# Kernel optimization log

Measured on AMD Instinct MI355X. Metric: run time of the kernel, lower is better.

## Reference

```python
import jax, jax.numpy as jnp
import numpy as np

B, N, D, H, DK, DV, HID = 4, 16384, 512, 8, 64, 64, 2048
LN_EPS = 1e-5   # torch nn.LayerNorm default
ATTN_EPS = 1e-6 # eps passed to LinearMultiHeadAttention


def _ln(h, g, b):
    m = jnp.mean(h, axis=-1, keepdims=True)
    v = jnp.mean(jnp.square(h - m), axis=-1, keepdims=True)
    return (h - m) * jax.lax.rsqrt(v + LN_EPS) * g + b


def setup_inputs() -> dict:
    key = jax.random.key(0)
    ks = jax.random.split(key, 8)
    w = lambda k, *sh: (jax.random.normal(k, sh, jnp.float32) * 0.02)
    return {
        "x": jax.random.normal(ks[0], (B, N, D), jnp.float32),
        "ln1_g": jnp.ones((D,), jnp.float32), "ln1_b": jnp.zeros((D,), jnp.float32),
        "Wq": w(ks[1], D, H * DK), "bq": jnp.zeros((H * DK,), jnp.float32),
        "Wk": w(ks[2], D, H * DK), "bk": jnp.zeros((H * DK,), jnp.float32),
        "Wv": w(ks[3], D, H * DV), "bv": jnp.zeros((H * DV,), jnp.float32),
        "Wo": w(ks[4], H * DV, D), "bo": jnp.zeros((D,), jnp.float32),
        "ln2_g": jnp.ones((D,), jnp.float32), "ln2_b": jnp.zeros((D,), jnp.float32),
        "W1": w(ks[5], D, HID), "b1": jnp.zeros((HID,), jnp.float32),
        "W2": w(ks[6], HID, D), "b2": jnp.zeros((D,), jnp.float32),
    }


def reference(x, ln1_g, ln1_b, Wq, bq, Wk, bk, Wv, bv, Wo, bo,
              ln2_g, ln2_b, W1, b1, W2, b2):
    # pre-LN (zero-width label concat is a no-op in label_embedded mode)
    h = _ln(x, ln1_g, ln1_b)                         # [B,N,D]
    q = (h @ Wq + bq).reshape(B, N, H, DK)
    k = (h @ Wk + bk).reshape(B, N, H, DK)
    v = (h @ Wv + bv).reshape(B, N, H, DV)
    # linear attention: phi = elu + 1 feature map, O(N) non-causal form
    pq = jax.nn.elu(q) + 1.0
    pk = jax.nn.elu(k) + 1.0
    kv = jnp.einsum('bnhd,bnhm->bhdm', pk, v)        # [B,H,DK,DV]
    ksum = jnp.sum(pk, axis=1)                       # [B,H,DK]
    z = 1.0 / (jnp.einsum('bnhd,bhd->bnh', pq, ksum) + ATTN_EPS)
    attn = jnp.einsum('bnhd,bhdm->bnhm', pq, kv) * z[..., None]
    attn = attn.reshape(B, N, H * DV) @ Wo + bo      # output projection
    h = h + attn                                     # residual 1
    h2 = _ln(h, ln2_g, ln2_b)
    dense = jax.nn.gelu(h2 @ W1 + b1) @ W2 + b2      # MLP, gelu activation
    return h2 + dense                                # residual 2
```

## Files before the change

### kernel.cpp

```cpp
#include <hip/hip_runtime.h>
#include <stdint.h>

#define BB   4
#define NN   16384
#define HH   8
#define DD   512
#define HIDN 2048
#define ROWST (BB * NN)

using short8 = __attribute__((ext_vector_type(8))) short;
using f32x4  = __attribute__((ext_vector_type(4))) float;

__device__ __forceinline__ float bf2f(uint16_t h) {
  union { uint32_t u; float f; } v; v.u = ((uint32_t)h) << 16; return v.f;
}
__device__ __forceinline__ uint16_t f2bf(float f) {
  union { float f; uint32_t u; } v; v.f = f;
  return (uint16_t)((v.u + 0x7FFFu + ((v.u >> 16) & 1u)) >> 16);
}
__device__ __forceinline__ float gelu_f(float x) {
  const float t1 = x * x;
  const float inner = __builtin_fmaf(0.044715f * t1, x, x);
  const float e = __expf(-1.5957691216f * inner);
  return x * __builtin_amdgcn_rcpf(1.f + e);
}
__device__ __forceinline__ void cp16(const uint16_t* g, uint16_t* l) {
  __builtin_amdgcn_global_load_lds((const __attribute__((address_space(1))) void*)g,
                                   (__attribute__((address_space(3))) void*)l, 16, 0, 0);
}
__device__ __forceinline__ int swz(int row, int col) {
  return row * 64 + (col ^ (row & 56));
}

template <int E>
__launch_bounds__(256)
__global__ void gemm_bt(const uint16_t* __restrict__ A, const uint16_t* __restrict__ BT,
                        const float* __restrict__ bias, const uint16_t* __restrict__ res,
                        void* __restrict__ outp, int M, int N, int K) {
  __shared__ __align__(16) uint16_t S[128 * 128];
  uint16_t* As = S;
  uint16_t* Bs = S + 128 * 64;
  const int tid = threadIdx.x;
  const int lane = tid & 63, wave = tid >> 6;
  const int l15 = lane & 15, l4 = lane >> 4;
  const int m0 = blockIdx.y * 128, n0 = blockIdx.x * 128;
  const int wm = (wave >> 1) * 64, wn = (wave & 1) * 64;

  f32x4 acc[4][4];
#pragma unroll
  for (int i = 0; i < 4; ++i)
#pragma unroll
    for (int j = 0; j < 4; ++j) acc[i][j] = (f32x4){0.f, 0.f, 0.f, 0.f};

  const int srow = tid >> 3;
  const int skc  = ((tid & 7) ^ (srow & 7)) * 8;
  const uint16_t* ga = A  + (size_t)(m0 + srow) * K + skc;
  const uint16_t* gb = BT + (size_t)(n0 + srow) * K + skc;

  for (int kb = 0; kb < K; kb += 64) {
    __syncthreads();
#pragma unroll
    for (int i = 0; i < 4; ++i) {
      cp16(ga + (size_t)i * 32 * K + kb, &As[(i * 256 + wave * 64) * 8]);
      cp16(gb + (size_t)i * 32 * K + kb, &Bs[(i * 256 + wave * 64) * 8]);
    }
    __syncthreads();
#pragma unroll
    for (int kk = 0; kk < 64; kk += 32) {
      short8 af[4], bfr[4];
#pragma unroll
      for (int i = 0; i < 4; ++i)
        af[i] = *(const short8*)&As[(wm + i * 16 + l15) * 64 +
                                    ((((kk >> 3) + l4) ^ (l15 & 7)) * 8)];
#pragma unroll
      for (int j = 0; j < 4; ++j)
        bfr[j] = *(const short8*)&Bs[(wn + j * 16 + l15) * 64 +
                                     ((((kk >> 3) + l4) ^ (l15 & 7)) * 8)];
#pragma unroll
      for (int i = 0; i < 4; ++i)
#pragma unroll
        for (int j = 0; j < 4; ++j)
          acc[i][j] = __builtin_amdgcn_mfma_f32_16x16x32_bf16(af[i], bfr[j], acc[i][j], 0, 0, 0);
    }
  }

  __syncthreads();
#pragma unroll
  for (int i = 0; i < 4; ++i)
#pragma unroll
    for (int r = 0; r < 4; ++r) {
      const int lrow = wm + i * 16 + l4 * 4 + r;
#pragma unroll
      for (int j = 0; j < 4; ++j) {
        const int lcol = wn + j * 16 + l15;
        float v = acc[i][j][r] + bias[n0 + lcol];
        if (E == 5) {
          if (n0 + lcol < 1024) v = v > 0.f ? v + 1.f : __expf(v);
        } else if (E == 3) {
          v = gelu_f(v);
        }
        S[lrow * 128 + ((((lcol >> 3) ^ (lrow >> 2)) & 15) * 8) + (lcol & 7)] = f2bf(v);
      }
    }
  __syncthreads();

  uint16_t* outb = (uint16_t*)outp;
  float* outf = (float*)outp;
  const int rr = tid >> 4;
  const int cb = tid & 15;
#pragma unroll
  for (int p = 0; p < 8; ++p) {
    const int lrow = p * 16 + rr;
    const int row = m0 + lrow;
    const int col0 = n0 + cb * 8;
    const uint4 d = *(const uint4*)&S[lrow * 128 + ((cb ^ (lrow >> 2)) & 15) * 8];
    if (E == 5) {
      const size_t off = (size_t)(col0 >> 9) * ((size_t)ROWST * DD) +
                         (size_t)row * DD + (col0 & 511);
      *(uint4*)&outb[off] = d;
    } else if (E == 1 || E == 3) {
      *(uint4*)&outb[(size_t)row * N + col0] = d;
    } else {
      const size_t idx = (size_t)row * N + col0;
      const uint4 rd = *(const uint4*)&res[idx];
      float a[8];
      a[0] = bf2f((uint16_t)(d.x & 0xffff)) + bf2f((uint16_t)(rd.x & 0xffff));
      a[1] = bf2f((uint16_t)(d.x >> 16))    + bf2f((uint16_t)(rd.x >> 16));
      a[2] = bf2f((uint16_t)(d.y & 0xffff)) + bf2f((uint16_t)(rd.y & 0xffff));
      a[3] = bf2f((uint16_t)(d.y >> 16))    + bf2f((uint16_t)(rd.y >> 16));
      a[4] = bf2f((uint16_t)(d.z & 0xffff)) + bf2f((uint16_t)(rd.z & 0xffff));
      a[5] = bf2f((uint16_t)(d.z >> 16))    + bf2f((uint16_t)(rd.z >> 16));
      a[6] = bf2f((uint16_t)(d.w & 0xffff)) + bf2f((uint16_t)(rd.w & 0xffff));
      a[7] = bf2f((uint16_t)(d.w >> 16))    + bf2f((uint16_t)(rd.w >> 16));
      if (E == 2) {
        uint4 o;
        o.x = (uint32_t)f2bf(a[0]) | ((uint32_t)f2bf(a[1]) << 16);
        o.y = (uint32_t)f2bf(a[2]) | ((uint32_t)f2bf(a[3]) << 16);
        o.z = (uint32_t)f2bf(a[4]) | ((uint32_t)f2bf(a[5]) << 16);
        o.w = (uint32_t)f2bf(a[6]) | ((uint32_t)f2bf(a[7]) << 16);
        *(uint4*)&outb[idx] = o;
      } else {
        *(float4*)&outf[idx]     = (float4){a[0], a[1], a[2], a[3]};
        *(float4*)&outf[idx + 4] = (float4){a[4], a[5], a[6], a[7]};
      }
    }
  }
}

template <int BFIN>
__launch_bounds__(256)
__global__ void ln_kernel(const void* __restrict__ inp, const float* __restrict__ gam,
                          const float* __restrict__ bet, uint16_t* __restrict__ out) {
  const int row = blockIdx.x * 4 + (threadIdx.x >> 6);
  const int lane = threadIdx.x & 63;
  const size_t base = (size_t)row * DD + lane * 8;
  float x[8];
  if (BFIN) {
    const uint4 u = *(const uint4*)((const uint16_t*)inp + base);
    x[0] = bf2f((uint16_t)(u.x & 0xffff)); x[1] = bf2f((uint16_t)(u.x >> 16));
    x[2] = bf2f((uint16_t)(u.y & 0xffff)); x[3] = bf2f((uint16_t)(u.y >> 16));
    x[4] = bf2f((uint16_t)(u.z & 0xffff)); x[5] = bf2f((uint16_t)(u.z >> 16));
    x[6] = bf2f((uint16_t)(u.w & 0xffff)); x[7] = bf2f((uint16_t)(u.w >> 16));
  } else {
    const float* f = (const float*)inp + base;
    const float4 a = *(const float4*)f;
    const float4 b = *(const float4*)(f + 4);
    x[0]=a.x; x[1]=a.y; x[2]=a.z; x[3]=a.w; x[4]=b.x; x[5]=b.y; x[6]=b.z; x[7]=b.w;
  }
  float s = 0.f, s2 = 0.f;
#pragma unroll
  for (int j = 0; j < 8; ++j) { s += x[j]; s2 += x[j] * x[j]; }
#pragma unroll
  for (int off = 32; off; off >>= 1) { s += __shfl_xor(s, off, 64); s2 += __shfl_xor(s2, off, 64); }
  const float m = s * (1.f / DD);
  const float rs = rsqrtf(s2 * (1.f / DD) - m * m + 1e-5f);
  uint16_t o[8];
#pragma unroll
  for (int j = 0; j < 8; ++j) {
    const int col = lane * 8 + j;
    o[j] = f2bf((x[j] - m) * rs * gam[col] + bet[col]);
  }
  uint4 w;
  w.x = (uint32_t)o[0] | ((uint32_t)o[1] << 16);
  w.y = (uint32_t)o[2] | ((uint32_t)o[3] << 16);
  w.z = (uint32_t)o[4] | ((uint32_t)o[5] << 16);
  w.w = (uint32_t)o[6] | ((uint32_t)o[7] << 16);
  *(uint4*)(out + base) = w;
}

__launch_bounds__(256)
__global__ void transpose_bf(const float* __restrict__ in, uint16_t* __restrict__ out,
                             int R, int C) {
  __shared__ float tile[32][33];
  const int tx = threadIdx.x, ty = threadIdx.y;
  const int c0 = blockIdx.x * 32, r0 = blockIdx.y * 32;
#pragma unroll
  for (int i = 0; i < 32; i += 8)
    tile[ty + i][tx] = in[(size_t)(r0 + ty + i) * C + (c0 + tx)];
  __syncthreads();
#pragma unroll
  for (int i = 0; i < 32; i += 8)
    out[(size_t)(c0 + ty + i) * R + (r0 + tx)] = f2bf(tile[tx][ty + i]);
}

__global__ void concat_bias(const float* __restrict__ bq, const float* __restrict__ bk,
                            const float* __restrict__ bv, float* __restrict__ o) {
  const int t = blockIdx.x * 256 + threadIdx.x;
  if (t < 512) o[t] = bq[t];
  else if (t < 1024) o[t] = bk[t - 512];
  else if (t < 1536) o[t] = bv[t - 1024];
}

__launch_bounds__(256)
__global__ void kv_mfma(const uint16_t* __restrict__ pk, const uint16_t* __restrict__ v,
                        float* __restrict__ kvp, float* __restrict__ ksp) {
  __shared__ __align__(16) uint16_t sT[4][2][64 * 64];
  __shared__ float ksred[64];
  const int bh = blockIdx.x, b = bh >> 3, h = bh & 7;
  const int t = threadIdx.x, lane = t & 63, w = t >> 6;
  const int l15 = lane & 15, l4 = lane >> 4;
  if (t < 64) ksred[t] = 0.f;
  __syncthreads();

  f32x4 acc[4][4];
#pragma unroll
  for (int i = 0; i < 4; ++i)
#pragma unroll
    for (int j = 0; j < 4; ++j) acc[i][j] = (f32x4){0.f, 0.f, 0.f, 0.f};
  float ks[4] = {0.f, 0.f, 0.f, 0.f};

  const int rl = lane >> 3, cl = (lane & 7) * 8;
  for (int sc = 0; sc < 4; ++sc) {
    const int nbase = blockIdx.y * 1024 + w * 256 + sc * 64;
#pragma unroll
    for (int ro = 0; ro < 8; ++ro) {
      const int n = ro * 8 + rl;
      const size_t gofs = ((size_t)(b * NN + nbase + n) * HH + h) * 64 + cl;
      const short8 pv = *(const short8*)(pk + gofs);
      const short8 vv = *(const short8*)(v + gofs);
#pragma unroll
      for (int j = 0; j < 8; ++j) {
        sT[w][0][swz(cl + j, n)] = (uint16_t)pv[j];
        sT[w][1][swz(cl + j, n)] = (uint16_t)vv[j];
      }
    }
#pragma unroll
    for (int kk = 0; kk < 64; kk += 32) {
      short8 af[4], bfr[4];
#pragma unroll
      for (int i = 0; i < 4; ++i)
        af[i] = *(const short8*)&sT[w][0][swz(i * 16 + l15, kk + l4 * 8)];
#pragma unroll
      for (int j = 0; j < 4; ++j)
        bfr[j] = *(const short8*)&sT[w][1][swz(j * 16 + l15, kk + l4 * 8)];
#pragma unroll
      for (int i = 0; i < 4; ++i) {
#pragma unroll
        for (int e = 0; e < 8; ++e) ks[i] += bf2f((uint16_t)af[i][e]);
#pragma unroll
        for (int j = 0; j < 4; ++j)
          acc[i][j] = __builtin_amdgcn_mfma_f32_16x16x32_bf16(af[i], bfr[j], acc[i][j], 0, 0, 0);
      }
    }
  }
#pragma unroll
  for (int i = 0; i < 4; ++i) {
    float s = ks[i];
    s += __shfl_xor(s, 16, 64); s += __shfl_xor(s, 32, 64);
    if (l4 == 0) atomicAdd(&ksred[i * 16 + l15], s);
  }
  __syncthreads();
  float* red = (float*)&sT[0][0][0];
  if (w > 0) {
#pragma unroll
    for (int i = 0; i < 4; ++i)
#pragma unroll
      for (int r = 0; r < 4; ++r)
#pragma unroll
        for (int j = 0; j < 4; ++j)
          red[(w - 1) * 4096 + (i * 16 + l4 * 4 + r) * 64 + j * 16 + l15] = acc[i][j][r];
  }
  __syncthreads();
  if (w == 0) {
    float* dst = kvp + ((size_t)bh * 16 + blockIdx.y) * 4096;
#pragma unroll
    for (int i = 0; i < 4; ++i)
#pragma unroll
      for (int r = 0; r < 4; ++r)
#pragma unroll
        for (int j = 0; j < 4; ++j) {
          const int e = (i * 16 + l4 * 4 + r) * 64 + j * 16 + l15;
          dst[e] = acc[i][j][r] + red[e] + red[4096 + e] + red[8192 + e];
        }
  }
  if (t < 64) ksp[((size_t)bh * 16 + blockIdx.y) * 64 + t] = ksred[t];
}

__launch_bounds__(256)
__global__ void kv_reduce(const float* __restrict__ kvp, const float* __restrict__ ksp,
                          float* __restrict__ kv, float* __restrict__ ksum) {
  const int bh = blockIdx.x;
  if (blockIdx.y == 16) {
    if (threadIdx.x < 64) {
      float s = 0.f;
      for (int c = 0; c < 16; ++c) s += ksp[((size_t)bh * 16 + c) * 64 + threadIdx.x];
      ksum[bh * 64 + threadIdx.x] = s;
    }
    return;
  }
  const int e = blockIdx.y * 256 + threadIdx.x;
  float s = 0.f;
  for (int c = 0; c < 16; ++c) s += kvp[((size_t)bh * 16 + c) * 4096 + e];
  kv[(size_t)bh * 4096 + e] = s;
}

__launch_bounds__(256)
__global__ void attn_mfma(const uint16_t* __restrict__ pq, const float* __restrict__ kv,
                          const float* __restrict__ ksum, uint16_t* __restrict__ attn) {
  __shared__ __align__(16) uint16_t kvT[64 * 64];
  __shared__ float ksS[64];
  __shared__ float denS[4][64];
  const int bh = blockIdx.x, b = bh >> 3, h = bh & 7;
  const int t = threadIdx.x, lane = t & 63, w = t >> 6;
  const int l15 = lane & 15, l4 = lane >> 4;
  const float* kvb = kv + (size_t)bh * 4096;
#pragma unroll
  for (int u = 0; u < 16; ++u) {
    const int e = u * 256 + t;
    kvT[swz(e & 63, e >> 6)] = f2bf(kvb[e]);
  }
  if (t < 64) ksS[t] = ksum[bh * 64 + t];
  __syncthreads();

  float ksr[16];
#pragma unroll
  for (int kk2 = 0; kk2 < 2; ++kk2) {
    const float4 k0 = *(const float4*)&ksS[kk2 * 32 + l4 * 8];
    const float4 k1 = *(const float4*)&ksS[kk2 * 32 + l4 * 8 + 4];
    ksr[kk2 * 8 + 0] = k0.x; ksr[kk2 * 8 + 1] = k0.y; ksr[kk2 * 8 + 2] = k0.z; ksr[kk2 * 8 + 3] = k0.w;
    ksr[kk2 * 8 + 4] = k1.x; ksr[kk2 * 8 + 5] = k1.y; ksr[kk2 * 8 + 6] = k1.z; ksr[kk2 * 8 + 7] = k1.w;
  }
  short8 bfrg[2][4];
#pragma unroll
  for (int kk2 = 0; kk2 < 2; ++kk2)
#pragma unroll
    for (int j = 0; j < 4; ++j)
      bfrg[kk2][j] = *(const short8*)&kvT[swz(j * 16 + l15, kk2 * 32 + l4 * 8)];

  const int n0w = blockIdx.y * 256 + w * 64;
  f32x4 acc[4][4];
#pragma unroll
  for (int i = 0; i < 4; ++i)
#pragma unroll
    for (int j = 0; j < 4; ++j) acc[i][j] = (f32x4){0.f, 0.f, 0.f, 0.f};
  float den[4] = {0.f, 0.f, 0.f, 0.f};

#pragma unroll
  for (int i = 0; i < 4; ++i) {
    const int n = n0w + i * 16 + l15;
    const size_t abase = ((size_t)(b * NN + n) * HH + h) * 64 + l4 * 8;
#pragma unroll
    for (int kk2 = 0; kk2 < 2; ++kk2) {
      const short8 af = *(const short8*)(pq + abase + kk2 * 32);
#pragma unroll
      for (int e = 0; e < 8; ++e) den[i] += bf2f((uint16_t)af[e]) * ksr[kk2 * 8 + e];
#pragma unroll
      for (int j = 0; j < 4; ++j)
        acc[i][j] = __builtin_amdgcn_mfma_f32_16x16x32_bf16(af, bfrg[kk2][j], acc[i][j], 0, 0, 0);
    }
  }
#pragma unroll
  for (int i = 0; i < 4; ++i) {
    float s = den[i];
    s += __shfl_xor(s, 16, 64); s += __shfl_xor(s, 32, 64);
    if (l4 == 0) denS[w][i * 16 + l15] = s;
  }
#pragma unroll
  for (int i = 0; i < 4; ++i)
#pragma unroll
    for (int r = 0; r < 4; ++r) {
      const float z = 1.f / (denS[w][i * 16 + l4 * 4 + r] + 1e-6f);
      const int n = n0w + i * 16 + l4 * 4 + r;
      const size_t ob = ((size_t)(b * NN + n) * HH + h) * 64;
#pragma unroll
      for (int j = 0; j < 4; ++j)
        attn[ob + j * 16 + l15] = f2bf(acc[i][j][r] * z);
    }
}

extern "C" void kernel_launch(void* const* d_in, const int* in_sizes, int n_in,
                              void* d_out, int out_size, void* d_ws, size_t ws_size,
                              hipStream_t stream) {
  (void)in_sizes; (void)n_in; (void)out_size;
  const float* x    = (const float*)d_in[0];
  const float* ln1g = (const float*)d_in[1];
  const float* ln1b = (const float*)d_in[2];
  const float* Wq   = (const float*)d_in[3];
  const float* bq   = (const float*)d_in[4];
  const float* Wk   = (const float*)d_in[5];
  const float* bk   = (const float*)d_in[6];
  const float* Wv   = (const float*)d_in[7];
  const float* bv   = (const float*)d_in[8];
  const float* Wo   = (const float*)d_in[9];
  const float* bo   = (const float*)d_in[10];
  const float* ln2g = (const float*)d_in[11];
  const float* ln2b = (const float*)d_in[12];
  const float* W1   = (const float*)d_in[13];
  const float* b1   = (const float*)d_in[14];
  const float* W2   = (const float*)d_in[15];
  const float* b2   = (const float*)d_in[16];

  if (ws_size < 409000000ULL) return;

  char* p = (char*)d_ws;
  auto alloc = [&](size_t bytes) -> char* {
    char* r = p; p += (bytes + 255) & ~(size_t)255; return r;
  };
  uint16_t* Hb  = (uint16_t*)alloc((size_t)ROWST * DD * 2);
  uint16_t* PQ  = (uint16_t*)alloc((size_t)ROWST * DD * 2);
  uint16_t* PK  = (uint16_t*)alloc((size_t)ROWST * DD * 2);
  uint16_t* PV  = (uint16_t*)alloc((size_t)ROWST * DD * 2);
  uint16_t* U   = (uint16_t*)alloc((size_t)32768 * HIDN * 2);
  uint16_t* WqkvT = (uint16_t*)alloc((size_t)1536 * DD * 2);
  uint16_t* WoT = (uint16_t*)alloc((size_t)DD * DD * 2);
  uint16_t* W1T = (uint16_t*)alloc((size_t)HIDN * DD * 2);
  uint16_t* W2T = (uint16_t*)alloc((size_t)DD * HIDN * 2);
  float*    bqkv = (float*)alloc(1536 * 4);
  float* KVP = (float*)U;
  float* KSP = KVP + 512 * 4096;
  float* KV  = KSP + 512 * 64;
  float* KS  = KV + 32 * 4096;

  const dim3 tb(32, 8);
  transpose_bf<<<dim3(16, 16), tb, 0, stream>>>(Wq, WqkvT, DD, DD);
  transpose_bf<<<dim3(16, 16), tb, 0, stream>>>(Wk, WqkvT + 512 * 512, DD, DD);
  transpose_bf<<<dim3(16, 16), tb, 0, stream>>>(Wv, WqkvT + 2 * 512 * 512, DD, DD);
  transpose_bf<<<dim3(16, 16), tb, 0, stream>>>(Wo, WoT, DD, DD);
  transpose_bf<<<dim3(64, 16), tb, 0, stream>>>(W1, W1T, DD, HIDN);
  transpose_bf<<<dim3(16, 64), tb, 0, stream>>>(W2, W2T, HIDN, DD);
  concat_bias<<<6, 256, 0, stream>>>(bq, bk, bv, bqkv);

  ln_kernel<0><<<ROWST / 4, 256, 0, stream>>>(x, ln1g, ln1b, Hb);
  gemm_bt<5><<<dim3(12, 512), 256, 0, stream>>>(Hb, WqkvT, bqkv, nullptr, PQ, ROWST, 1536, DD);
  kv_mfma<<<dim3(32, 16), 256, 0, stream>>>(PK, PV, KVP, KSP);
  kv_reduce<<<dim3(32, 17), 256, 0, stream>>>(KVP, KSP, KV, KS);
  attn_mfma<<<dim3(32, 64), 256, 0, stream>>>(PQ, KV, KS, PV);
  gemm_bt<2><<<dim3(4, 512), 256, 0, stream>>>(PV, WoT, bo, Hb, PK, ROWST, DD, DD);
  ln_kernel<1><<<ROWST / 4, 256, 0, stream>>>(PK, ln2g, ln2b, PQ);
  for (int c = 0; c < 2; ++c) {
    const uint16_t* h2c = PQ + (size_t)c * 32768 * DD;
    gemm_bt<3><<<dim3(16, 256), 256, 0, stream>>>(h2c, W1T, b1, nullptr, U, 32768, HIDN, DD);
    gemm_bt<4><<<dim3(4, 256), 256, 0, stream>>>(U, W2T, b2, h2c,
        (float*)d_out + (size_t)c * 32768 * DD, 32768, DD, HIDN);
  }
}
```

Baseline: 1.037 ms.

## Replace GEMM with 256x128 triple-buffered pipelined kernel and XCD-aware tile remap

The 128x128 single-buffered GEMM is replaced by a 512-thread, 256x128-tile kernel that keeps three LDS stages and issues the global-to-LDS loads two k-steps ahead, using explicit waitcnt and barriers. MFMA blocks get raised wave priority, and workgroup IDs are remapped so consecutive tiles land on the same XCD for better L2 reuse. The goal is to hide load latency behind MFMA work and cut synchronisation per k-step. In exchange it uses much more LDS (144KB per block) and relies on hand-placed vmcnt counts being correct.

```diff
diff --git a/kernel.cpp b/kernel.cpp
--- a/kernel.cpp
+++ b/kernel.cpp
@@ -33,67 +33,97 @@
 }
 
 template <int E>
-__launch_bounds__(256)
-__global__ void gemm_bt(const uint16_t* __restrict__ A, const uint16_t* __restrict__ BT,
+__launch_bounds__(512, 2)
+__global__ void gemm256(const uint16_t* __restrict__ A, const uint16_t* __restrict__ BT,
                         const float* __restrict__ bias, const uint16_t* __restrict__ res,
                         void* __restrict__ outp, int M, int N, int K) {
-  __shared__ __align__(16) uint16_t S[128 * 128];
-  uint16_t* As = S;
-  uint16_t* Bs = S + 128 * 64;
+  __shared__ __align__(16) uint16_t S[3 * 24576];
   const int tid = threadIdx.x;
   const int lane = tid & 63, wave = tid >> 6;
   const int l15 = lane & 15, l4 = lane >> 4;
-  const int m0 = blockIdx.y * 128, n0 = blockIdx.x * 128;
   const int wm = (wave >> 1) * 64, wn = (wave & 1) * 64;
 
+  const int gx = gridDim.x;
+  const int nwg = gx * gridDim.y;
+  const int orig = blockIdx.y * gx + blockIdx.x;
+  const int q = nwg >> 3, r = nwg & 7;
+  const int xcd = orig & 7, off = orig >> 3;
+  const int tile = (xcd < r ? xcd * (q + 1) : r * (q + 1) + (xcd - r) * q) + off;
+  const int tn = tile % gx, tm = tile / gx;
+  const int m0 = tm * 256, n0 = tn * 128;
+
+  uint16_t *A0 = S,             *B0 = S + 16384;
+  uint16_t *A1 = S + 24576,     *B1 = S + 40960;
+  uint16_t *A2 = S + 49152,     *B2 = S + 65536;
+
+  const int srow = tid >> 3;
+  const int scb  = (tid & 7) ^ (srow & 7);
+  const uint16_t* ga = A  + (size_t)(m0 + srow) * K + scb * 8;
+  const uint16_t* gb = BT + (size_t)(n0 + srow) * K + scb * 8;
+  auto stage = [&](uint16_t* Ad, uint16_t* Bd, int kb) {
+#pragma unroll
+    for (int r2 = 0; r2 < 4; ++r2)
+      cp16(ga + (size_t)r2 * 64 * K + kb, Ad + (r2 * 64 + wave * 8) * 64);
+#pragma unroll
+    for (int r2 = 0; r2 < 2; ++r2)
+      cp16(gb + (size_t)r2 * 64 * K + kb, Bd + (r2 * 64 + wave * 8) * 64);
+  };
+
   f32x4 acc[4][4];
 #pragma unroll
   for (int i = 0; i < 4; ++i)
 #pragma unroll
     for (int j = 0; j < 4; ++j) acc[i][j] = (f32x4){0.f, 0.f, 0.f, 0.f};
 
-  const int srow = tid >> 3;
-  const int skc  = ((tid & 7) ^ (srow & 7)) * 8;
-  const uint16_t* ga = A  + (size_t)(m0 + srow) * K + skc;
-  const uint16_t* gb = BT + (size_t)(n0 + srow) * K + skc;
-
-  for (int kb = 0; kb < K; kb += 64) {
-    __syncthreads();
-#pragma unroll
-    for (int i = 0; i < 4; ++i) {
-      cp16(ga + (size_t)i * 32 * K + kb, &As[(i * 256 + wave * 64) * 8]);
-      cp16(gb + (size_t)i * 32 * K + kb, &Bs[(i * 256 + wave * 64) * 8]);
-    }
-    __syncthreads();
-#pragma unroll
-    for (int kk = 0; kk < 64; kk += 32) {
-      short8 af[4], bfr[4];
+  const int NT = K >> 6;
+  stage(A0, B0, 0);
+  stage(A1, B1, 64);
+  asm volatile("s_waitcnt vmcnt(6)" ::: "memory");
+  __builtin_amdgcn_s_barrier();
+  asm volatile("" ::: "memory");
+
+  for (int t = 0; t < NT; ++t) {
+    short8 af[2][4], bfr[2][4];
+#pragma unroll
+    for (int h = 0; h < 2; ++h) {
 #pragma unroll
       for (int i = 0; i < 4; ++i)
-        af[i] = *(const short8*)&As[(wm + i * 16 + l15) * 64 +
-                                    ((((kk >> 3) + l4) ^ (l15 & 7)) * 8)];
+        af[h][i] = *(const short8*)&A0[(wm + i * 16 + l15) * 64 +
+                                       (((h * 4 + l4) ^ (l15 & 7)) * 8)];
 #pragma unroll
       for (int j = 0; j < 4; ++j)
-        bfr[j] = *(const short8*)&Bs[(wn + j * 16 + l15) * 64 +
-                                     ((((kk >> 3) + l4) ^ (l15 & 7)) * 8)];
+        bfr[h][j] = *(const short8*)&B0[(wn + j * 16 + l15) * 64 +
+                                        (((h * 4 + l4) ^ (l15 & 7)) * 8)];
+    }
+    if (t + 2 < NT) stage(A2, B2, (t + 2) << 6);
+#pragma unroll
+    for (int h = 0; h < 2; ++h) {
+      __builtin_amdgcn_s_setprio(1);
 #pragma unroll
       for (int i = 0; i < 4; ++i)
 #pragma unroll
         for (int j = 0; j < 4; ++j)
-          acc[i][j] = __builtin_amdgcn_mfma_f32_16x16x32_bf16(af[i], bfr[j], acc[i][j], 0, 0, 0);
-    }
-  }
-
-  __syncthreads();
+          acc[i][j] = __builtin_amdgcn_mfma_f32_16x16x32_bf16(af[h][i], bfr[h][j],
+                                                              acc[i][j], 0, 0, 0);
+      __builtin_amdgcn_s_setprio(0);
+    }
+    if (t + 2 < NT) asm volatile("s_waitcnt vmcnt(6) lgkmcnt(0)" ::: "memory");
+    else            asm volatile("s_waitcnt vmcnt(0) lgkmcnt(0)" ::: "memory");
+    __builtin_amdgcn_s_barrier();
+    asm volatile("" ::: "memory");
+    uint16_t* tA = A0; A0 = A1; A1 = A2; A2 = tA;
+    uint16_t* tB = B0; B0 = B1; B1 = B2; B2 = tB;
+  }
+
 #pragma unroll
   for (int i = 0; i < 4; ++i)
 #pragma unroll
-    for (int r = 0; r < 4; ++r) {
-      const int lrow = wm + i * 16 + l4 * 4 + r;
+    for (int rg = 0; rg < 4; ++rg) {
+      const int lrow = wm + i * 16 + l4 * 4 + rg;
 #pragma unroll
       for (int j = 0; j < 4; ++j) {
         const int lcol = wn + j * 16 + l15;
-        float v = acc[i][j][r] + bias[n0 + lcol];
+        float v = acc[i][j][rg] + bias[n0 + lcol];
         if (E == 5) {
           if (n0 + lcol < 1024) v = v > 0.f ? v + 1.f : __expf(v);
         } else if (E == 3) {
@@ -110,14 +140,14 @@
   const int cb = tid & 15;
 #pragma unroll
   for (int p = 0; p < 8; ++p) {
-    const int lrow = p * 16 + rr;
+    const int lrow = p * 32 + rr;
     const int row = m0 + lrow;
     const int col0 = n0 + cb * 8;
     const uint4 d = *(const uint4*)&S[lrow * 128 + ((cb ^ (lrow >> 2)) & 15) * 8];
     if (E == 5) {
-      const size_t off = (size_t)(col0 >> 9) * ((size_t)ROWST * DD) +
-                         (size_t)row * DD + (col0 & 511);
-      *(uint4*)&outb[off] = d;
+      const size_t offs = (size_t)(col0 >> 9) * ((size_t)ROWST * DD) +
+                          (size_t)row * DD + (col0 & 511);
+      *(uint4*)&outb[offs] = d;
     } else if (E == 1 || E == 3) {
       *(uint4*)&outb[(size_t)row * N + col0] = d;
     } else {
@@ -441,16 +471,16 @@
   concat_bias<<<6, 256, 0, stream>>>(bq, bk, bv, bqkv);
 
   ln_kernel<0><<<ROWST / 4, 256, 0, stream>>>(x, ln1g, ln1b, Hb);
-  gemm_bt<5><<<dim3(12, 512), 256, 0, stream>>>(Hb, WqkvT, bqkv, nullptr, PQ, ROWST, 1536, DD);
+  gemm256<5><<<dim3(12, 256), 512, 0, stream>>>(Hb, WqkvT, bqkv, nullptr, PQ, ROWST, 1536, DD);
   kv_mfma<<<dim3(32, 16), 256, 0, stream>>>(PK, PV, KVP, KSP);
   kv_reduce<<<dim3(32, 17), 256, 0, stream>>>(KVP, KSP, KV, KS);
   attn_mfma<<<dim3(32, 64), 256, 0, stream>>>(PQ, KV, KS, PV);
-  gemm_bt<2><<<dim3(4, 512), 256, 0, stream>>>(PV, WoT, bo, Hb, PK, ROWST, DD, DD);
+  gemm256<2><<<dim3(4, 256), 512, 0, stream>>>(PV, WoT, bo, Hb, PK, ROWST, DD, DD);
   ln_kernel<1><<<ROWST / 4, 256, 0, stream>>>(PK, ln2g, ln2b, PQ);
   for (int c = 0; c < 2; ++c) {
     const uint16_t* h2c = PQ + (size_t)c * 32768 * DD;
-    gemm_bt<3><<<dim3(16, 256), 256, 0, stream>>>(h2c, W1T, b1, nullptr, U, 32768, HIDN, DD);
-    gemm_bt<4><<<dim3(4, 256), 256, 0, stream>>>(U, W2T, b2, h2c,
+    gemm256<3><<<dim3(16, 128), 512, 0, stream>>>(h2c, W1T, b1, nullptr, U, 32768, HIDN, DD);
+    gemm256<4><<<dim3(4, 128), 512, 0, stream>>>(U, W2T, b2, h2c,
         (float*)d_out + (size_t)c * 32768 * DD, 32768, DD, HIDN);
   }
 }
```

New measurement: 980.0 us. 5.5% less time.

## Replace 128x128 GEMM with 256x256 double-buffered ping-pong MFMA kernel

Applied to the files above, without the earlier changes.

Replaces the 128x128-tile, 4-wave GEMM with a 256x256-tile, 8-wave kernel. It double-buffers global-to-LDS loads in half-K phases interleaved with MFMA bursts under s_setprio and explicit barriers, and remaps workgroup IDs so tiles are grouped in chunks of eight. The larger tile raises arithmetic intensity per LDS byte, and the software pipeline is meant to hide global load latency behind compute. It uses 128 KB of LDS and many accumulator registers, which could limit occupancy, and the hand-tuned waitcnt scheme depends on K being a multiple of 128.

```diff
diff --git a/kernel.cpp b/kernel.cpp
--- a/kernel.cpp
+++ b/kernel.cpp
@@ -33,91 +33,154 @@
 }
 
 template <int E>
-__launch_bounds__(256)
-__global__ void gemm_bt(const uint16_t* __restrict__ A, const uint16_t* __restrict__ BT,
+__launch_bounds__(512, 2)
+__global__ void gemm256(const uint16_t* __restrict__ A, const uint16_t* __restrict__ BT,
                         const float* __restrict__ bias, const uint16_t* __restrict__ res,
                         void* __restrict__ outp, int M, int N, int K) {
-  __shared__ __align__(16) uint16_t S[128 * 128];
-  uint16_t* As = S;
-  uint16_t* Bs = S + 128 * 64;
+  __shared__ __align__(16) uint16_t S[65536];
   const int tid = threadIdx.x;
   const int lane = tid & 63, wave = tid >> 6;
   const int l15 = lane & 15, l4 = lane >> 4;
-  const int m0 = blockIdx.y * 128, n0 = blockIdx.x * 128;
-  const int wm = (wave >> 1) * 64, wn = (wave & 1) * 64;
-
-  f32x4 acc[4][4];
-#pragma unroll
-  for (int i = 0; i < 4; ++i)
+  const int wm = (wave >> 2) * 128, wn = (wave & 3) * 64;
+
+  const int gx = gridDim.x;
+  const int nwg = gx * gridDim.y;
+  const int orig = blockIdx.y * gx + blockIdx.x;
+  const int cpx = nwg >> 3;
+  const int tile = (orig & 7) * cpx + (orig >> 3);
+  const int tn = tile % gx, tm = tile / gx;
+  const int m0 = tm * 256, n0 = tn * 256;
+
+  const int bsw = (tid & 7) ^ ((tid >> 3) & 7);
+  const int row_lo = ((tid >> 3) << 1) + (bsw >> 2);
+  const int c8 = (bsw & 3) * 8;
+  const uint16_t* pA = A  + (size_t)(m0 + row_lo) * K + c8;
+  const uint16_t* pB = BT + (size_t)(n0 + row_lo) * K + c8;
+  const size_t rstep = (size_t)128 * K;
+  const int dstw = wave * 512;
+
+  const int pbF = (((l15 & 1) << 2) | l4) ^ (l15 >> 1);
+  const int abase = wm * 32 + (l15 >> 1) * 64 + pbF * 8;
+  const int bbase = 16384 + wn * 32 + (l15 >> 1) * 64 + pbF * 8;
+
+  auto stageA = [&](int buf, int kh, int kb) {
+    uint16_t* d = S + buf * 32768 + kh * 8192 + dstw;
+    const uint16_t* s = pA + kb + kh * 32;
+    cp16(s, d);
+    cp16(s + rstep, d + 4096);
+  };
+  auto stageB = [&](int buf, int kh, int kb) {
+    uint16_t* d = S + buf * 32768 + 16384 + kh * 8192 + dstw;
+    const uint16_t* s = pB + kb + kh * 32;
+    cp16(s, d);
+    cp16(s + rstep, d + 4096);
+  };
+
+  f32x4 acc[8][4];
+#pragma unroll
+  for (int i = 0; i < 8; ++i)
 #pragma unroll
     for (int j = 0; j < 4; ++j) acc[i][j] = (f32x4){0.f, 0.f, 0.f, 0.f};
-
-  const int srow = tid >> 3;
-  const int skc  = ((tid & 7) ^ (srow & 7)) * 8;
-  const uint16_t* ga = A  + (size_t)(m0 + srow) * K + skc;
-  const uint16_t* gb = BT + (size_t)(n0 + srow) * K + skc;
-
-  for (int kb = 0; kb < K; kb += 64) {
-    __syncthreads();
-#pragma unroll
-    for (int i = 0; i < 4; ++i) {
-      cp16(ga + (size_t)i * 32 * K + kb, &As[(i * 256 + wave * 64) * 8]);
-      cp16(gb + (size_t)i * 32 * K + kb, &Bs[(i * 256 + wave * 64) * 8]);
-    }
-    __syncthreads();
-#pragma unroll
-    for (int kk = 0; kk < 64; kk += 32) {
-      short8 af[4], bfr[4];
-#pragma unroll
-      for (int i = 0; i < 4; ++i)
-        af[i] = *(const short8*)&As[(wm + i * 16 + l15) * 64 +
-                                    ((((kk >> 3) + l4) ^ (l15 & 7)) * 8)];
-#pragma unroll
-      for (int j = 0; j < 4; ++j)
-        bfr[j] = *(const short8*)&Bs[(wn + j * 16 + l15) * 64 +
-                                     ((((kk >> 3) + l4) ^ (l15 & 7)) * 8)];
-#pragma unroll
-      for (int i = 0; i < 4; ++i)
-#pragma unroll
-        for (int j = 0; j < 4; ++j)
-          acc[i][j] = __builtin_amdgcn_mfma_f32_16x16x32_bf16(af[i], bfr[j], acc[i][j], 0, 0, 0);
-    }
-  }
-
-  __syncthreads();
-#pragma unroll
-  for (int i = 0; i < 4; ++i)
-#pragma unroll
-    for (int r = 0; r < 4; ++r) {
-      const int lrow = wm + i * 16 + l4 * 4 + r;
+  short8 bf[4];
+
+  const int NT = K >> 6;
+  stageA(0, 0, 0);  stageB(0, 0, 0);
+  stageA(0, 1, 0);  stageB(0, 1, 0);
+  stageA(1, 0, 64); stageB(1, 0, 64);
+  asm volatile("s_waitcnt vmcnt(4)" ::: "memory");
+  __builtin_amdgcn_s_barrier();
+  asm volatile("" ::: "memory");
+
+#define PHASE(BUF, MH, KH, RB, PRE, POST)                                        \
+  {                                                                              \
+    short8 af[4];                                                                \
+    _Pragma("unroll")                                                            \
+    for (int f = 0; f < 4; ++f)                                                  \
+      af[f] = *(const short8*)&S[(BUF)*32768 + (KH)*8192 + (MH)*2048 + abase + f*512]; \
+    if (RB) {                                                                    \
+      _Pragma("unroll")                                                          \
+      for (int j = 0; j < 4; ++j)                                                \
+        bf[j] = *(const short8*)&S[(BUF)*32768 + (KH)*8192 + bbase + j*512];     \
+    }                                                                            \
+    PRE;                                                                         \
+    asm volatile("" ::: "memory");                                               \
+    __builtin_amdgcn_s_barrier();                                                \
+    asm volatile("s_waitcnt lgkmcnt(0)" ::: "memory");                           \
+    __builtin_amdgcn_sched_barrier(0);                                           \
+    __builtin_amdgcn_s_setprio(1);                                               \
+    _Pragma("unroll")                                                            \
+    for (int i = 0; i < 4; ++i)                                                  \
+      _Pragma("unroll")                                                          \
+      for (int j = 0; j < 4; ++j)                                                \
+        acc[(MH)*4 + i][j] = __builtin_amdgcn_mfma_f32_16x16x32_bf16(af[i], bf[j], acc[(MH)*4 + i][j], 0, 0, 0); \
+    __builtin_amdgcn_s_setprio(0);                                               \
+    __builtin_amdgcn_sched_barrier(0);                                           \
+    POST;                                                                        \
+    asm volatile("" ::: "memory");                                               \
+    __builtin_amdgcn_s_barrier();                                                \
+    asm volatile("" ::: "memory");                                               \
+  }
+
+  for (int t2 = 0; t2 < NT; t2 += 2) {
+    {
+      const int t = t2;
+      const int kb1 = (t + 1) << 6, kb2 = (t + 2) << 6;
+      PHASE(0, 0, 0, 1, if (t + 1 < NT) stageA(1, 1, kb1), {});
+      PHASE(0, 1, 0, 0, if (t + 1 < NT) stageB(1, 1, kb1), {});
+      PHASE(0, 0, 1, 1, if (t + 2 < NT) stageA(0, 0, kb2), {});
+      PHASE(0, 1, 1, 0, if (t + 2 < NT) stageB(0, 0, kb2),
+            if (t + 2 < NT) { asm volatile("s_waitcnt vmcnt(4)" ::: "memory"); }
+            else            { asm volatile("s_waitcnt vmcnt(0)" ::: "memory"); });
+    }
+    {
+      const int t = t2 + 1;
+      const int kb1 = (t + 1) << 6, kb2 = (t + 2) << 6;
+      PHASE(1, 0, 0, 1, if (t + 1 < NT) stageA(0, 1, kb1), {});
+      PHASE(1, 1, 0, 0, if (t + 1 < NT) stageB(0, 1, kb1), {});
+      PHASE(1, 0, 1, 1, if (t + 2 < NT) stageA(1, 0, kb2), {});
+      PHASE(1, 1, 1, 0, if (t + 2 < NT) stageB(1, 0, kb2),
+            if (t + 2 < NT) { asm volatile("s_waitcnt vmcnt(4)" ::: "memory"); }
+            else            { asm volatile("s_waitcnt vmcnt(0)" ::: "memory"); });
+    }
+  }
+#undef PHASE
+
+  __syncthreads();
+  const float bj[4] = {bias[n0 + wn + l15], bias[n0 + wn + 16 + l15],
+                       bias[n0 + wn + 32 + l15], bias[n0 + wn + 48 + l15]};
+#pragma unroll
+  for (int mf = 0; mf < 8; ++mf)
+#pragma unroll
+    for (int rg = 0; rg < 4; ++rg) {
+      const int lrow = wm + mf * 16 + l4 * 4 + rg;
 #pragma unroll
       for (int j = 0; j < 4; ++j) {
         const int lcol = wn + j * 16 + l15;
-        float v = acc[i][j][r] + bias[n0 + lcol];
+        float v = acc[mf][j][rg] + bj[j];
         if (E == 5) {
           if (n0 + lcol < 1024) v = v > 0.f ? v + 1.f : __expf(v);
         } else if (E == 3) {
           v = gelu_f(v);
         }
-        S[lrow * 128 + ((((lcol >> 3) ^ (lrow >> 2)) & 15) * 8) + (lcol & 7)] = f2bf(v);
+        S[lrow * 256 + ((((lcol >> 3) ^ lrow) & 31) * 8) + (lcol & 7)] = f2bf(v);
       }
     }
   __syncthreads();
 
   uint16_t* outb = (uint16_t*)outp;
   float* outf = (float*)outp;
-  const int rr = tid >> 4;
-  const int cb = tid & 15;
-#pragma unroll
-  for (int p = 0; p < 8; ++p) {
+  const int rr = tid >> 5;
+  const int cb = tid & 31;
+#pragma unroll
+  for (int p = 0; p < 16; ++p) {
     const int lrow = p * 16 + rr;
     const int row = m0 + lrow;
     const int col0 = n0 + cb * 8;
-    const uint4 d = *(const uint4*)&S[lrow * 128 + ((cb ^ (lrow >> 2)) & 15) * 8];
+    const uint4 d = *(const uint4*)&S[lrow * 256 + ((cb ^ lrow) & 31) * 8];
     if (E == 5) {
-      const size_t off = (size_t)(col0 >> 9) * ((size_t)ROWST * DD) +
-                         (size_t)row * DD + (col0 & 511);
-      *(uint4*)&outb[off] = d;
+      const size_t offs = (size_t)(col0 >> 9) * ((size_t)ROWST * DD) +
+                          (size_t)row * DD + (col0 & 511);
+      *(uint4*)&outb[offs] = d;
     } else if (E == 1 || E == 3) {
       *(uint4*)&outb[(size_t)row * N + col0] = d;
     } else {
@@ -441,16 +504,16 @@
   concat_bias<<<6, 256, 0, stream>>>(bq, bk, bv, bqkv);
 
   ln_kernel<0><<<ROWST / 4, 256, 0, stream>>>(x, ln1g, ln1b, Hb);
-  gemm_bt<5><<<dim3(12, 512), 256, 0, stream>>>(Hb, WqkvT, bqkv, nullptr, PQ, ROWST, 1536, DD);
+  gemm256<5><<<dim3(6, 256), 512, 0, stream>>>(Hb, WqkvT, bqkv, nullptr, PQ, ROWST, 1536, DD);
   kv_mfma<<<dim3(32, 16), 256, 0, stream>>>(PK, PV, KVP, KSP);
   kv_reduce<<<dim3(32, 17), 256, 0, stream>>>(KVP, KSP, KV, KS);
   attn_mfma<<<dim3(32, 64), 256, 0, stream>>>(PQ, KV, KS, PV);
-  gemm_bt<2><<<dim3(4, 512), 256, 0, stream>>>(PV, WoT, bo, Hb, PK, ROWST, DD, DD);
+  gemm256<2><<<dim3(2, 256), 512, 0, stream>>>(PV, WoT, bo, Hb, PK, ROWST, DD, DD);
   ln_kernel<1><<<ROWST / 4, 256, 0, stream>>>(PK, ln2g, ln2b, PQ);
   for (int c = 0; c < 2; ++c) {
     const uint16_t* h2c = PQ + (size_t)c * 32768 * DD;
-    gemm_bt<3><<<dim3(16, 256), 256, 0, stream>>>(h2c, W1T, b1, nullptr, U, 32768, HIDN, DD);
-    gemm_bt<4><<<dim3(4, 256), 256, 0, stream>>>(U, W2T, b2, h2c,
+    gemm256<3><<<dim3(8, 128), 512, 0, stream>>>(h2c, W1T, b1, nullptr, U, 32768, HIDN, DD);
+    gemm256<4><<<dim3(2, 128), 512, 0, stream>>>(U, W2T, b2, h2c,
         (float*)d_out + (size_t)c * 32768 * DD, 32768, DD, HIDN);
   }
 }
```

New measurement: 959.2 us. 1.08x faster.

## Replace GEMM with 256x128 double-buffered tile kernel and remapped block order

Applied to the files above, without the earlier changes.

Replaces the 128x128 single-buffered GEMM with a 256x128 tile kernel that double-buffers 32-wide K slices in LDS, so the next slice is loaded while MFMAs run on the current one. Each wave now holds a 128x64 accumulator block, raising register pressure. Launch bounds ask for two blocks per CU. Block indices are permuted across groups of eight, likely to improve L2 locality across XCDs. The epilogue is staged through LDS in two halves with bias preloaded into registers.

```diff
diff --git a/kernel.cpp b/kernel.cpp
--- a/kernel.cpp
+++ b/kernel.cpp
@@ -33,117 +33,139 @@
 }
 
 template <int E>
-__launch_bounds__(256)
-__global__ void gemm_bt(const uint16_t* __restrict__ A, const uint16_t* __restrict__ BT,
+__launch_bounds__(256, 2)
+__global__ void gemm256(const uint16_t* __restrict__ A, const uint16_t* __restrict__ BT,
                         const float* __restrict__ bias, const uint16_t* __restrict__ res,
                         void* __restrict__ outp, int M, int N, int K) {
-  __shared__ __align__(16) uint16_t S[128 * 128];
-  uint16_t* As = S;
-  uint16_t* Bs = S + 128 * 64;
+  __shared__ __align__(16) uint16_t S[24576];
   const int tid = threadIdx.x;
   const int lane = tid & 63, wave = tid >> 6;
   const int l15 = lane & 15, l4 = lane >> 4;
-  const int m0 = blockIdx.y * 128, n0 = blockIdx.x * 128;
-  const int wm = (wave >> 1) * 64, wn = (wave & 1) * 64;
-
-  f32x4 acc[4][4];
-#pragma unroll
-  for (int i = 0; i < 4; ++i)
+  const int wm = ((wave >> 1) & 1) * 128, wn = (wave & 1) * 64;
+
+  const int gx = gridDim.x;
+  const int nwg = gx * gridDim.y;
+  const int orig = blockIdx.y * gx + blockIdx.x;
+  const int cpx = nwg >> 3;
+  const int tile = (orig & 7) * cpx + (orig >> 3);
+  const int tn = tile % gx, tm = tile / gx;
+  const int m0 = tm * 256, n0 = tn * 128;
+
+  const int pbl = (tid & 7) ^ ((tid >> 3) & 7);
+  const int arow = ((tid >> 3) << 1) + (pbl >> 2);
+  const int kcb8 = (pbl & 3) * 8;
+  const uint16_t* pA = A  + (size_t)(m0 + arow) * K + kcb8;
+  const uint16_t* pB = BT + (size_t)(n0 + arow) * K + kcb8;
+  const size_t rstep = (size_t)64 * K;
+
+  auto stage = [&](int buf, int kb) {
+    uint16_t* Ad = S + buf * 12288;
+    uint16_t* Bd = Ad + 8192;
+#pragma unroll
+    for (int r = 0; r < 4; ++r)
+      cp16(pA + kb + r * rstep, Ad + (r * 256 + tid) * 8);
+#pragma unroll
+    for (int r = 0; r < 2; ++r)
+      cp16(pB + kb + r * rstep, Bd + (r * 256 + tid) * 8);
+  };
+
+  const int pbF = (((l15 & 1) << 2) | l4) ^ (l15 >> 1);
+  const int aidx0 = ((wm + l15) >> 1) * 64 + pbF * 8;
+  const int bidx0 = 8192 + ((wn + l15) >> 1) * 64 + pbF * 8;
+
+  f32x4 acc[8][4];
+#pragma unroll
+  for (int i = 0; i < 8; ++i)
 #pragma unroll
     for (int j = 0; j < 4; ++j) acc[i][j] = (f32x4){0.f, 0.f, 0.f, 0.f};
 
-  const int srow = tid >> 3;
-  const int skc  = ((tid & 7) ^ (srow & 7)) * 8;
-  const uint16_t* ga = A  + (size_t)(m0 + srow) * K + skc;
-  const uint16_t* gb = BT + (size_t)(n0 + srow) * K + skc;
-
-  for (int kb = 0; kb < K; kb += 64) {
+  stage(0, 0);
+  __syncthreads();
+  int buf = 0;
+  for (int kb = 0; kb < K; kb += 32) {
+    if (kb + 32 < K) stage(buf ^ 1, kb + 32);
+    const int ab = buf * 12288 + aidx0;
+    const int bb = buf * 12288 + bidx0;
+    short8 bfr[4];
+#pragma unroll
+    for (int j = 0; j < 4; ++j) bfr[j] = *(const short8*)&S[bb + j * 512];
+#pragma unroll
+    for (int mf = 0; mf < 8; ++mf) {
+      const short8 af = *(const short8*)&S[ab + mf * 512];
+#pragma unroll
+      for (int j = 0; j < 4; ++j)
+        acc[mf][j] = __builtin_amdgcn_mfma_f32_16x16x32_bf16(af, bfr[j], acc[mf][j], 0, 0, 0);
+    }
     __syncthreads();
-#pragma unroll
-    for (int i = 0; i < 4; ++i) {
-      cp16(ga + (size_t)i * 32 * K + kb, &As[(i * 256 + wave * 64) * 8]);
-      cp16(gb + (size_t)i * 32 * K + kb, &Bs[(i * 256 + wave * 64) * 8]);
-    }
-    __syncthreads();
-#pragma unroll
-    for (int kk = 0; kk < 64; kk += 32) {
-      short8 af[4], bfr[4];
-#pragma unroll
-      for (int i = 0; i < 4; ++i)
-        af[i] = *(const short8*)&As[(wm + i * 16 + l15) * 64 +
-                                    ((((kk >> 3) + l4) ^ (l15 & 7)) * 8)];
-#pragma unroll
-      for (int j = 0; j < 4; ++j)
-        bfr[j] = *(const short8*)&Bs[(wn + j * 16 + l15) * 64 +
-                                     ((((kk >> 3) + l4) ^ (l15 & 7)) * 8)];
-#pragma unroll
-      for (int i = 0; i < 4; ++i)
-#pragma unroll
-        for (int j = 0; j < 4; ++j)
-          acc[i][j] = __builtin_amdgcn_mfma_f32_16x16x32_bf16(af[i], bfr[j], acc[i][j], 0, 0, 0);
-    }
-  }
-
-  __syncthreads();
-#pragma unroll
-  for (int i = 0; i < 4; ++i)
-#pragma unroll
-    for (int r = 0; r < 4; ++r) {
-      const int lrow = wm + i * 16 + l4 * 4 + r;
-#pragma unroll
-      for (int j = 0; j < 4; ++j) {
-        const int lcol = wn + j * 16 + l15;
-        float v = acc[i][j][r] + bias[n0 + lcol];
-        if (E == 5) {
-          if (n0 + lcol < 1024) v = v > 0.f ? v + 1.f : __expf(v);
-        } else if (E == 3) {
-          v = gelu_f(v);
-        }
-        S[lrow * 128 + ((((lcol >> 3) ^ (lrow >> 2)) & 15) * 8) + (lcol & 7)] = f2bf(v);
-      }
-    }
-  __syncthreads();
+    buf ^= 1;
+  }
 
   uint16_t* outb = (uint16_t*)outp;
   float* outf = (float*)outp;
+  const float bj[4] = {bias[n0 + wn + l15], bias[n0 + wn + 16 + l15],
+                       bias[n0 + wn + 32 + l15], bias[n0 + wn + 48 + l15]};
   const int rr = tid >> 4;
   const int cb = tid & 15;
 #pragma unroll
-  for (int p = 0; p < 8; ++p) {
-    const int lrow = p * 16 + rr;
-    const int row = m0 + lrow;
-    const int col0 = n0 + cb * 8;
-    const uint4 d = *(const uint4*)&S[lrow * 128 + ((cb ^ (lrow >> 2)) & 15) * 8];
-    if (E == 5) {
-      const size_t off = (size_t)(col0 >> 9) * ((size_t)ROWST * DD) +
-                         (size_t)row * DD + (col0 & 511);
-      *(uint4*)&outb[off] = d;
-    } else if (E == 1 || E == 3) {
-      *(uint4*)&outb[(size_t)row * N + col0] = d;
-    } else {
-      const size_t idx = (size_t)row * N + col0;
-      const uint4 rd = *(const uint4*)&res[idx];
-      float a[8];
-      a[0] = bf2f((uint16_t)(d.x & 0xffff)) + bf2f((uint16_t)(rd.x & 0xffff));
-      a[1] = bf2f((uint16_t)(d.x >> 16))    + bf2f((uint16_t)(rd.x >> 16));
-      a[2] = bf2f((uint16_t)(d.y & 0xffff)) + bf2f((uint16_t)(rd.y & 0xffff));
-      a[3] = bf2f((uint16_t)(d.y >> 16))    + bf2f((uint16_t)(rd.y >> 16));
-      a[4] = bf2f((uint16_t)(d.z & 0xffff)) + bf2f((uint16_t)(rd.z & 0xffff));
-      a[5] = bf2f((uint16_t)(d.z >> 16))    + bf2f((uint16_t)(rd.z >> 16));
-      a[6] = bf2f((uint16_t)(d.w & 0xffff)) + bf2f((uint16_t)(rd.w & 0xffff));
-      a[7] = bf2f((uint16_t)(d.w >> 16))    + bf2f((uint16_t)(rd.w >> 16));
-      if (E == 2) {
-        uint4 o;
-        o.x = (uint32_t)f2bf(a[0]) | ((uint32_t)f2bf(a[1]) << 16);
-        o.y = (uint32_t)f2bf(a[2]) | ((uint32_t)f2bf(a[3]) << 16);
-        o.z = (uint32_t)f2bf(a[4]) | ((uint32_t)f2bf(a[5]) << 16);
-        o.w = (uint32_t)f2bf(a[6]) | ((uint32_t)f2bf(a[7]) << 16);
-        *(uint4*)&outb[idx] = o;
+  for (int mh = 0; mh < 2; ++mh) {
+    if (wm == mh * 128) {
+#pragma unroll
+      for (int mf = 0; mf < 8; ++mf)
+#pragma unroll
+        for (int rg = 0; rg < 4; ++rg) {
+          const int lrow = mf * 16 + l4 * 4 + rg;
+#pragma unroll
+          for (int j = 0; j < 4; ++j) {
+            const int lcol = wn + j * 16 + l15;
+            float v = acc[mf][j][rg] + bj[j];
+            if (E == 5) {
+              if (n0 + lcol < 1024) v = v > 0.f ? v + 1.f : __expf(v);
+            } else if (E == 3) {
+              v = gelu_f(v);
+            }
+            S[lrow * 128 + ((((lcol >> 3) ^ lrow) & 15) * 8) + (lcol & 7)] = f2bf(v);
+          }
+        }
+    }
+    __syncthreads();
+#pragma unroll
+    for (int p = 0; p < 8; ++p) {
+      const int lrow = p * 16 + rr;
+      const int row = m0 + mh * 128 + lrow;
+      const int col0 = n0 + cb * 8;
+      const uint4 d = *(const uint4*)&S[lrow * 128 + ((cb ^ lrow) & 15) * 8];
+      if (E == 5) {
+        const size_t offs = (size_t)(col0 >> 9) * ((size_t)ROWST * DD) +
+                            (size_t)row * DD + (col0 & 511);
+        *(uint4*)&outb[offs] = d;
+      } else if (E == 1 || E == 3) {
+        *(uint4*)&outb[(size_t)row * N + col0] = d;
       } else {
-        *(float4*)&outf[idx]     = (float4){a[0], a[1], a[2], a[3]};
-        *(float4*)&outf[idx + 4] = (float4){a[4], a[5], a[6], a[7]};
+        const size_t idx = (size_t)row * N + col0;
+        const uint4 rd = *(const uint4*)&res[idx];
+        float a[8];
+        a[0] = bf2f((uint16_t)(d.x & 0xffff)) + bf2f((uint16_t)(rd.x & 0xffff));
+        a[1] = bf2f((uint16_t)(d.x >> 16))    + bf2f((uint16_t)(rd.x >> 16));
+        a[2] = bf2f((uint16_t)(d.y & 0xffff)) + bf2f((uint16_t)(rd.y & 0xffff));
+        a[3] = bf2f((uint16_t)(d.y >> 16))    + bf2f((uint16_t)(rd.y >> 16));
+        a[4] = bf2f((uint16_t)(d.z & 0xffff)) + bf2f((uint16_t)(rd.z & 0xffff));
+        a[5] = bf2f((uint16_t)(d.z >> 16))    + bf2f((uint16_t)(rd.z >> 16));
+        a[6] = bf2f((uint16_t)(d.w & 0xffff)) + bf2f((uint16_t)(rd.w & 0xffff));
+        a[7] = bf2f((uint16_t)(d.w >> 16))    + bf2f((uint16_t)(rd.w >> 16));
+        if (E == 2) {
+          uint4 o;
+          o.x = (uint32_t)f2bf(a[0]) | ((uint32_t)f2bf(a[1]) << 16);
+          o.y = (uint32_t)f2bf(a[2]) | ((uint32_t)f2bf(a[3]) << 16);
+          o.z = (uint32_t)f2bf(a[4]) | ((uint32_t)f2bf(a[5]) << 16);
+          o.w = (uint32_t)f2bf(a[6]) | ((uint32_t)f2bf(a[7]) << 16);
+          *(uint4*)&outb[idx] = o;
+        } else {
+          *(float4*)&outf[idx]     = (float4){a[0], a[1], a[2], a[3]};
+          *(float4*)&outf[idx + 4] = (float4){a[4], a[5], a[6], a[7]};
+        }
       }
     }
+    if (mh == 0) __syncthreads();
   }
 }
 
@@ -441,16 +463,16 @@
   concat_bias<<<6, 256, 0, stream>>>(bq, bk, bv, bqkv);
 
   ln_kernel<0><<<ROWST / 4, 256, 0, stream>>>(x, ln1g, ln1b, Hb);
-  gemm_bt<5><<<dim3(12, 512), 256, 0, stream>>>(Hb, WqkvT, bqkv, nullptr, PQ, ROWST, 1536, DD);
+  gemm256<5><<<dim3(12, 256), 256, 0, stream>>>(Hb, WqkvT, bqkv, nullptr, PQ, ROWST, 1536, DD);
   kv_mfma<<<dim3(32, 16), 256, 0, stream>>>(PK, PV, KVP, KSP);
   kv_reduce<<<dim3(32, 17), 256, 0, stream>>>(KVP, KSP, KV, KS);
   attn_mfma<<<dim3(32, 64), 256, 0, stream>>>(PQ, KV, KS, PV);
-  gemm_bt<2><<<dim3(4, 512), 256, 0, stream>>>(PV, WoT, bo, Hb, PK, ROWST, DD, DD);
+  gemm256<2><<<dim3(4, 256), 256, 0, stream>>>(PV, WoT, bo, Hb, PK, ROWST, DD, DD);
   ln_kernel<1><<<ROWST / 4, 256, 0, stream>>>(PK, ln2g, ln2b, PQ);
   for (int c = 0; c < 2; ++c) {
     const uint16_t* h2c = PQ + (size_t)c * 32768 * DD;
-    gemm_bt<3><<<dim3(16, 256), 256, 0, stream>>>(h2c, W1T, b1, nullptr, U, 32768, HIDN, DD);
-    gemm_bt<4><<<dim3(4, 256), 256, 0, stream>>>(U, W2T, b2, h2c,
+    gemm256<3><<<dim3(16, 128), 256, 0, stream>>>(h2c, W1T, b1, nullptr, U, 32768, HIDN, DD);
+    gemm256<4><<<dim3(4, 128), 256, 0, stream>>>(U, W2T, b2, h2c,
         (float*)d_out + (size_t)c * 32768 * DD, 32768, DD, HIDN);
   }
 }
```

New measurement: 1.144 ms. 10.3% more time.
